# Performance work log

Hardware: AMD Instinct MI355X
Metric: run time of the kernel (lower is better)

The kernel has to match this reference:

```python
import jax, jax.numpy as jnp
import numpy as np

B, S, E, H = 4, 2048, 512, 8
D = E // H  # 64 per-head dim


def setup_inputs() -> dict:
    key = jax.random.key(0)
    kq, kk, kv, kwq, kwk, kwv, kwf, kbf = jax.random.split(key, 8)
    sc = 0.02
    return {
        "query": jax.random.normal(kq, (B, S, E), dtype=jnp.float32),
        "key": jax.random.normal(kk, (B, S, E), dtype=jnp.float32),
        "value": jax.random.normal(kv, (B, S, E), dtype=jnp.float32),
        "Wq": jax.random.normal(kwq, (D, D), dtype=jnp.float32) * sc,
        "Wk": jax.random.normal(kwk, (D, D), dtype=jnp.float32) * sc,
        "Wv": jax.random.normal(kwv, (D, D), dtype=jnp.float32) * sc,
        "Wfc": jax.random.normal(kwf, (E, E), dtype=jnp.float32) * sc,
        "bfc": jnp.zeros((E,), dtype=jnp.float32),
        "mask": jnp.tril(jnp.ones((1, 1, S, S), dtype=jnp.int32)),
    }


def reference(query, key, value, Wq, Wk, Wv, Wfc, bfc, mask):
    b, qlen, _ = query.shape
    klen = key.shape[1]
    # split heads: (B, L, H, D)
    q = query.reshape(b, qlen, H, D)
    k = key.reshape(b, klen, H, D)
    v = value.reshape(b, klen, H, D)
    # per-head linear projections (torch Linear: x @ W.T, no bias)
    q = jnp.einsum('bqhd,ed->bqhe', q, Wq)
    k = jnp.einsum('bkhd,ed->bkhe', k, Wk)
    v = jnp.einsum('bkhd,ed->bkhe', v, Wv)
    # full score matrix (B, H, Q, K)
    scores = jnp.einsum('bqhd,bkhd->bhqk', q, k)
    # faithful to source: mask-fill BEFORE dividing by sqrt(d)
    scores = jnp.where(mask == 0, jnp.float32(-1e20), scores)
    scores = scores / jnp.float32(np.sqrt(D))
    attn = jax.nn.softmax(scores, axis=-1)
    out = jnp.einsum('bhqk,bkhd->bqhd', attn, v).reshape(b, qlen, H * D)
    return out @ Wfc.T + bfc
```

## Files before the change

kernel.cpp:

```cpp
#include <hip/hip_runtime.h>
#include <hip/hip_bf16.h>

#define S_LEN 2048
#define EMB 512
#define NH 8
#define HD 64

#define AS1 __attribute__((address_space(1)))
#define AS3 __attribute__((address_space(3)))

typedef __bf16 bf16x8 __attribute__((ext_vector_type(8)));
typedef __bf16 bf16x4 __attribute__((ext_vector_type(4)));
typedef float f32x4 __attribute__((ext_vector_type(4)));
typedef float f32x16 __attribute__((ext_vector_type(16)));
typedef int i32x4 __attribute__((ext_vector_type(4)));

__device__ __forceinline__ unsigned swz(unsigned byteoff, unsigned row) {
    return byteoff ^ ((row & 7u) << 4);
}

__device__ __forceinline__ bf16x8 cvt8(const float* src) {
    float4 f0 = *reinterpret_cast<const float4*>(src);
    float4 f1 = *reinterpret_cast<const float4*>(src + 4);
    bf16x8 r;
    r[0] = (__bf16)f0.x; r[1] = (__bf16)f0.y; r[2] = (__bf16)f0.z; r[3] = (__bf16)f0.w;
    r[4] = (__bf16)f1.x; r[5] = (__bf16)f1.y; r[6] = (__bf16)f1.z; r[7] = (__bf16)f1.w;
    return r;
}

__global__ __launch_bounds__(256) void wcvt_kernel(
    const float* __restrict__ Wfc, const float* __restrict__ Wq,
    const float* __restrict__ Wk, const float* __restrict__ Wv,
    __bf16* __restrict__ Wb, __bf16* __restrict__ Wf)
{
    if (blockIdx.x < 128) {
        int i = (blockIdx.x * 256 + threadIdx.x) * 8;
        *reinterpret_cast<bf16x8*>(Wb + i) = cvt8(Wfc + i);
    } else {
        int s = (blockIdx.x - 128) * 256 + threadIdx.x;
        int p = s >> 9, rem = s & 511;
        int sub = rem >> 6, l = rem & 63;
        int nf = sub >> 1, ks = sub & 1;
        int col = l & 15, g = l >> 4;
        const float* Wsrc = (p == 0) ? Wq : (p == 1) ? Wk : Wv;
        *reinterpret_cast<bf16x8*>(Wf + (size_t)s * 8) =
            cvt8(Wsrc + (nf * 16 + col) * HD + ks * 32 + g * 8);
    }
}

__global__ __launch_bounds__(256) void proj_kernel(
    const float* __restrict__ qin, const float* __restrict__ kin, const float* __restrict__ vin,
    const __bf16* __restrict__ Wf,
    __bf16* __restrict__ Qf, __bf16* __restrict__ Kf, __bf16* __restrict__ Vf)
{
    __shared__ alignas(16) unsigned char xb[8192];
    __shared__ alignas(16) unsigned char tb[8192];
    const int p = blockIdx.z;
    const int bh = blockIdx.y;
    const int b = bh >> 3, h = bh & 7;
    const int sblk = blockIdx.x << 6;
    const int tid = threadIdx.x;
    const int w = tid >> 6, l = tid & 63;
    const int col = l & 15, g = l >> 4;
    const float K1 = 0.18033688011112042f;

    const float* src = (p == 0 ? qin : p == 1 ? kin : vin) +
                       ((size_t)b * S_LEN + sblk) * EMB + h * HD;
    #pragma unroll
    for (int it = 0; it < 4; ++it) {
        int c = tid + it * 256;
        int row = c >> 4, c4 = c & 15;
        float4 f = *reinterpret_cast<const float4*>(src + (size_t)row * EMB + c4 * 4);
        bf16x4 t;
        t[0] = (__bf16)f.x; t[1] = (__bf16)f.y; t[2] = (__bf16)f.z; t[3] = (__bf16)f.w;
        *reinterpret_cast<bf16x4*>(&xb[swz(row * 128 + c4 * 8, row)]) = t;
    }
    __syncthreads();

    bf16x8 wf[4][2];
    {
        const __bf16* wfb = Wf + p * 4096 + l * 8;
        #pragma unroll
        for (int nf = 0; nf < 4; ++nf)
            #pragma unroll
            for (int ks = 0; ks < 2; ++ks)
                wf[nf][ks] = *reinterpret_cast<const bf16x8*>(wfb + (nf * 2 + ks) * 512);
    }
    int arow = w * 16 + col;
    bf16x8 a0 = *reinterpret_cast<const bf16x8*>(&xb[swz(arow * 128 + g * 16, arow)]);
    bf16x8 a1 = *reinterpret_cast<const bf16x8*>(&xb[swz(arow * 128 + 64 + g * 16, arow)]);
    f32x4 acc[4];
    #pragma unroll
    for (int nf = 0; nf < 4; ++nf) acc[nf] = (f32x4){0.f, 0.f, 0.f, 0.f};
    #pragma unroll
    for (int nf = 0; nf < 4; ++nf) {
        acc[nf] = __builtin_amdgcn_mfma_f32_16x16x32_bf16(a0, wf[nf][0], acc[nf], 0, 0, 0);
        acc[nf] = __builtin_amdgcn_mfma_f32_16x16x32_bf16(a1, wf[nf][1], acc[nf], 0, 0, 0);
    }
    const float s0 = (p == 0) ? K1 : 1.0f;
    #pragma unroll
    for (int nf = 0; nf < 4; ++nf)
        #pragma unroll
        for (int r = 0; r < 4; ++r) {
            int srow = w * 16 + g * 4 + r;
            unsigned tba = (unsigned)(srow * 128 + (nf * 16 + col) * 2) ^ ((srow & 7u) << 4);
            *reinterpret_cast<__bf16*>(&tb[tba]) = (__bf16)(acc[nf][r] * s0);
        }
    __syncthreads();
    if (p < 2) {
        __bf16* dst = (p == 0) ? Qf : Kf;
        #pragma unroll
        for (int it = 0; it < 2; ++it) {
            int s = tid + it * 256;
            int Tloc = s >> 8, ks = (s >> 6) & 3, li = s & 63;
            int c32 = li & 31, h2 = li >> 5;
            int row = Tloc * 32 + c32;
            unsigned tba = (unsigned)(row * 128 + ks * 32 + h2 * 16) ^ ((row & 7u) << 4);
            bf16x8 v = *reinterpret_cast<const bf16x8*>(&tb[tba]);
            *reinterpret_cast<bf16x8*>(
                dst + (size_t)bh * 131072 +
                ((size_t)(blockIdx.x * 2 + Tloc) * 4 + ks) * 512 + li * 8) = v;
        }
    } else {
        #pragma unroll
        for (int it = 0; it < 2; ++it) {
            int s = tid + it * 256;
            int Tloc = s >> 8, sub = (s >> 6) & 3, li = s & 63;
            int nf = sub >> 1, ks2 = sub & 1;
            int c32 = li & 31, h2 = li >> 5;
            int dcol = nf * 32 + c32;
            bf16x8 v;
            #pragma unroll
            for (int e = 0; e < 8; ++e) {
                int row = Tloc * 32 + ks2 * 16 + (e & 3) + 8 * (e >> 2) + 4 * h2;
                unsigned tba = (unsigned)(row * 128 + dcol * 2) ^ ((row & 7u) << 4);
                v[e] = *reinterpret_cast<const __bf16*>(&tb[tba]);
            }
            *reinterpret_cast<bf16x8*>(
                Vf + (size_t)bh * 131072 +
                ((size_t)(blockIdx.x * 2 + Tloc) * 4 + sub) * 512 + li * 8) = v;
        }
    }
}

__global__ __launch_bounds__(256, 4) void attn_kernel(
    const __bf16* __restrict__ Qf, const __bf16* __restrict__ Kf,
    const __bf16* __restrict__ Vf, __bf16* __restrict__ Oa)
{
    __shared__ float mg[2][2112];
    const int l_id = blockIdx.x;
    const int bh = l_id & 31;
    const int pr = l_id >> 5;
    const int b = bh >> 3, h = bh & 7;
    const int tid = threadIdx.x;
    const int kh = tid >> 6;
    const int l = tid & 63;
    const int c32 = l & 31, hi = l >> 5;

    const __bf16* kbase = Kf + (size_t)bh * 131072;
    const __bf16* vbase = Vf + (size_t)bh * 131072;

    #pragma unroll 1
    for (int pass = 0; pass < 2; ++pass) {
        const int qt2 = pass ? 63 - pr : pr;

        bf16x8 qf[4];
        {
            const __bf16* qb = Qf + (size_t)bh * 131072 + (size_t)qt2 * 2048 + l * 8;
            #pragma unroll
            for (int ks = 0; ks < 4; ++ks)
                qf[ks] = *reinterpret_cast<const bf16x8*>(qb + ks * 512);
        }
        f32x16 oacc[2];
        #pragma unroll
        for (int nf = 0; nf < 2; ++nf)
            #pragma unroll
            for (int r = 0; r < 16; ++r) oacc[nf][r] = 0.f;
        float lsum = 0.f;

        const int cnt = (qt2 >= kh) ? ((qt2 - kh) >> 2) + 1 : 0;
        const bool has_mask = (kh == (qt2 & 3));
        const __bf16* kp = kbase + (size_t)kh * 2048 + l * 8;
        const __bf16* vp = vbase + (size_t)kh * 2048 + l * 8;

        #pragma unroll 1
        for (int i = 0; i < cnt; ++i) {
            bf16x8 kcur[4], vcur[4];
            #pragma unroll
            for (int j = 0; j < 4; ++j) {
                kcur[j] = *reinterpret_cast<const bf16x8*>(kp + j * 512);
                vcur[j] = *reinterpret_cast<const bf16x8*>(vp + j * 512);
            }
            f32x16 sfa;
            #pragma unroll
            for (int r = 0; r < 16; ++r) sfa[r] = -16.f;
            #pragma unroll
            for (int ks = 0; ks < 4; ++ks)
                sfa = __builtin_amdgcn_mfma_f32_32x32x16_bf16(kcur[ks], qf[ks], sfa, 0, 0, 0);
            if (has_mask && i == cnt - 1) {
                #pragma unroll
                for (int r = 0; r < 16; ++r) {
                    int kvloc = (r & 3) + 8 * (r >> 2) + 4 * hi;
                    if (kvloc > c32) sfa[r] = -1e30f;
                }
            }
            float rsum = 0.f;
            int wds[8];
            #pragma unroll
            for (int i2 = 0; i2 < 8; ++i2) {
                float p0 = __builtin_exp2f(sfa[2 * i2]);
                float p1 = __builtin_exp2f(sfa[2 * i2 + 1]);
                rsum += p0 + p1;
                asm("v_cvt_pk_bf16_f32 %0, %1, %2" : "=v"(wds[i2]) : "v"(p0), "v"(p1));
            }
            lsum += rsum;
            #pragma unroll
            for (int nf = 0; nf < 2; ++nf) {
                #pragma unroll
                for (int ks2 = 0; ks2 < 2; ++ks2) {
                    i32x4 pw;
                    pw[0] = wds[ks2 * 4 + 0];
                    pw[1] = wds[ks2 * 4 + 1];
                    pw[2] = wds[ks2 * 4 + 2];
                    pw[3] = wds[ks2 * 4 + 3];
                    bf16x8 pfk = *reinterpret_cast<bf16x8*>(&pw);
                    oacc[nf] = __builtin_amdgcn_mfma_f32_32x32x16_bf16(
                        vcur[nf * 2 + ks2], pfk, oacc[nf], 0, 0, 0);
                }
            }
            kp += 8192;
            vp += 8192;
        }

        __syncthreads();
        if (kh & 1) {
            float* bp = mg[kh >> 1];
            #pragma unroll
            for (int nf = 0; nf < 2; ++nf)
                #pragma unroll
                for (int r = 0; r < 16; ++r)
                    bp[(nf * 16 + r) * 64 + l] = oacc[nf][r];
            bp[2048 + l] = lsum;
        }
        __syncthreads();
        if (!(kh & 1)) {
            const float* bp = mg[kh >> 1];
            lsum += bp[2048 + l];
            #pragma unroll
            for (int nf = 0; nf < 2; ++nf)
                #pragma unroll
                for (int r = 0; r < 16; ++r)
                    oacc[nf][r] += bp[(nf * 16 + r) * 64 + l];
        }
        __syncthreads();
        if (kh == 2) {
            float* bp = mg[0];
            #pragma unroll
            for (int nf = 0; nf < 2; ++nf)
                #pragma unroll
                for (int r = 0; r < 16; ++r)
                    bp[(nf * 16 + r) * 64 + l] = oacc[nf][r];
            bp[2048 + l] = lsum;
        }
        __syncthreads();
        if (kh == 0) {
            const float* bp = mg[0];
            lsum += bp[2048 + l];
            #pragma unroll
            for (int nf = 0; nf < 2; ++nf)
                #pragma unroll
                for (int r = 0; r < 16; ++r)
                    oacc[nf][r] += bp[(nf * 16 + r) * 64 + l];
            lsum += __shfl_xor(lsum, 32);
            float inv = 1.0f / lsum;
            const int q = qt2 * 32 + c32;
            __bf16* op = Oa + ((size_t)b * S_LEN + q) * EMB + h * HD;
            #pragma unroll
            for (int nf = 0; nf < 2; ++nf)
                #pragma unroll
                for (int rq = 0; rq < 4; ++rq) {
                    bf16x4 o4;
                    #pragma unroll
                    for (int e = 0; e < 4; ++e)
                        o4[e] = (__bf16)(oacc[nf][rq * 4 + e] * inv);
                    *reinterpret_cast<bf16x4*>(op + nf * 32 + rq * 8 + hi * 4) = o4;
                }
        }
    }
}

__global__ __launch_bounds__(512) void fc_kernel(
    const __bf16* __restrict__ A,
    const __bf16* __restrict__ Wb,
    const float* __restrict__ bfc,
    float* __restrict__ out)
{
    __shared__ alignas(16) unsigned char smem[65536];
    const int tid = threadIdx.x;
    const int w = tid >> 6, l = tid & 63;
    const int c32 = l & 31, hi = l >> 5;
    const int mw = w >> 2, nw = w & 3;
    const int r0 = blockIdx.x * 128, n0 = blockIdx.y * 128;

    int sro[2], sof[2];
    #pragma unroll
    for (int j = 0; j < 2; ++j) {
        int s = w * 128 + j * 64 + l;
        int row = s >> 3, off = (s & 7) * 16;
        sro[j] = row;
        sof[j] = off ^ ((row & 7) << 4);
    }
    const unsigned char* Ag = reinterpret_cast<const unsigned char*>(A) + (size_t)r0 * 1024;
    const unsigned char* Wg = reinterpret_cast<const unsigned char*>(Wb) + (size_t)n0 * 1024;

    f32x16 oacc[2];
    #pragma unroll
    for (int nf = 0; nf < 2; ++nf)
        #pragma unroll
        for (int r = 0; r < 16; ++r) oacc[nf][r] = 0.f;

    #pragma unroll
    for (int j = 0; j < 2; ++j) {
        __builtin_amdgcn_global_load_lds(
            (const AS1 unsigned int*)(Ag + (size_t)sro[j] * 1024 + sof[j]),
            (AS3 unsigned int*)(smem + w * 2048 + j * 1024), 16, 0, 0);
        __builtin_amdgcn_global_load_lds(
            (const AS1 unsigned int*)(Wg + (size_t)sro[j] * 1024 + sof[j]),
            (AS3 unsigned int*)(smem + 16384 + w * 2048 + j * 1024), 16, 0, 0);
    }
    __syncthreads();

    int cur = 0;
    #pragma unroll 1
    for (int kc = 0; kc < 8; ++kc) {
        if (kc + 1 < 8) {
            unsigned char* Abn = smem + (cur ^ 1) * 32768;
            #pragma unroll
            for (int j = 0; j < 2; ++j) {
                __builtin_amdgcn_global_load_lds(
                    (const AS1 unsigned int*)(Ag + (size_t)sro[j] * 1024 + (kc + 1) * 128 + sof[j]),
                    (AS3 unsigned int*)(Abn + w * 2048 + j * 1024), 16, 0, 0);
                __builtin_amdgcn_global_load_lds(
                    (const AS1 unsigned int*)(Wg + (size_t)sro[j] * 1024 + (kc + 1) * 128 + sof[j]),
                    (AS3 unsigned int*)(Abn + 16384 + w * 2048 + j * 1024), 16, 0, 0);
            }
        }
        unsigned char* Ab = smem + cur * 32768;
        unsigned char* Wbuf = Ab + 16384;
        const int brow = nw * 32 + c32;
        #pragma unroll
        for (int ks = 0; ks < 4; ++ks) {
            bf16x8 bfg = *reinterpret_cast<const bf16x8*>(
                Wbuf + swz(brow * 128 + ks * 32 + hi * 16, brow));
            #pragma unroll
            for (int nf = 0; nf < 2; ++nf) {
                int arow = mw * 64 + nf * 32 + c32;
                bf16x8 afg = *reinterpret_cast<const bf16x8*>(
                    Ab + swz(arow * 128 + ks * 32 + hi * 16, arow));
                oacc[nf] = __builtin_amdgcn_mfma_f32_32x32x16_bf16(afg, bfg, oacc[nf], 0, 0, 0);
            }
        }
        __syncthreads();
        cur ^= 1;
    }

    const float bias = bfc[n0 + nw * 32 + c32];
    const int ncol = n0 + nw * 32 + c32;
    #pragma unroll
    for (int nf = 0; nf < 2; ++nf)
        #pragma unroll
        for (int r = 0; r < 16; ++r) {
            int mrow = r0 + mw * 64 + nf * 32 + (r & 3) + 8 * (r >> 2) + 4 * hi;
            out[(size_t)mrow * EMB + ncol] = oacc[nf][r] + bias;
        }
}

extern "C" void kernel_launch(void* const* d_in, const int* in_sizes, int n_in,
                              void* d_out, int out_size, void* d_ws, size_t ws_size,
                              hipStream_t stream) {
    const float* q   = (const float*)d_in[0];
    const float* k   = (const float*)d_in[1];
    const float* v   = (const float*)d_in[2];
    const float* Wq  = (const float*)d_in[3];
    const float* Wk  = (const float*)d_in[4];
    const float* Wv  = (const float*)d_in[5];
    const float* Wfc = (const float*)d_in[6];
    const float* bfc = (const float*)d_in[7];
    float* out = (float*)d_out;

    char* ws = (char*)d_ws;
    const size_t SZ = (size_t)4 * NH * S_LEN * HD * sizeof(__bf16);
    __bf16* Qf = (__bf16*)(ws);
    __bf16* Kf = (__bf16*)(ws + SZ);
    __bf16* Vf = (__bf16*)(ws + 2 * SZ);
    __bf16* Oa = (__bf16*)(ws + 3 * SZ);
    __bf16* Wb = (__bf16*)(ws + 4 * SZ);
    __bf16* Wf = (__bf16*)(ws + 4 * SZ + 524288);

    wcvt_kernel<<<dim3(134), 256, 0, stream>>>(Wfc, Wq, Wk, Wv, Wb, Wf);
    proj_kernel<<<dim3(S_LEN / 64, 4 * NH, 3), 256, 0, stream>>>(q, k, v, Wf, Qf, Kf, Vf);
    attn_kernel<<<dim3(32 * 32), 256, 0, stream>>>(Qf, Kf, Vf, Oa);
    fc_kernel<<<dim3((4 * S_LEN) / 128, EMB / 128), 512, 0, stream>>>(Oa, Wb, bfc, out);
}
```

Before: 66.45 us.

## Fuse paired causal query tiles into one KV loop sharing K/V loads

The attention kernel now processes both paired query tiles (pr and 63-pr) in a single loop over KV blocks instead of two sequential passes. Each loaded K/V fragment is reused for both tiles, roughly halving global K/V traffic for the shorter tile and removing a second loop prologue. This doubles Q-fragment and accumulator register use, so launch bounds drop from 4 to 3 waves per SIMD, which lowers occupancy and latency hiding. The merge/epilogue loop then indexes the two accumulator sets through a pointer, which may force register arrays into scratch memory.

```diff
diff --git a/kernel.cpp b/kernel.cpp
--- a/kernel.cpp
+++ b/kernel.cpp
@@ -143,7 +143,7 @@
     }
 }
 
-__global__ __launch_bounds__(256, 4) void attn_kernel(
+__global__ __launch_bounds__(256, 3) void attn_kernel(
     const __bf16* __restrict__ Qf, const __bf16* __restrict__ Kf,
     const __bf16* __restrict__ Vf, __bf16* __restrict__ Oa)
 {
@@ -157,81 +157,122 @@
     const int l = tid & 63;
     const int c32 = l & 31, hi = l >> 5;
 
-    const __bf16* kbase = Kf + (size_t)bh * 131072;
-    const __bf16* vbase = Vf + (size_t)bh * 131072;
+    const int qtA = pr, qtB = 63 - pr;
+
+    bf16x8 qfA[4], qfB[4];
+    {
+        const __bf16* qa = Qf + (size_t)bh * 131072 + (size_t)qtA * 2048 + l * 8;
+        const __bf16* qb = Qf + (size_t)bh * 131072 + (size_t)qtB * 2048 + l * 8;
+        #pragma unroll
+        for (int ks = 0; ks < 4; ++ks) {
+            qfA[ks] = *reinterpret_cast<const bf16x8*>(qa + ks * 512);
+            qfB[ks] = *reinterpret_cast<const bf16x8*>(qb + ks * 512);
+        }
+    }
+    f32x16 oaccA[2], oaccB[2];
+    #pragma unroll
+    for (int nf = 0; nf < 2; ++nf)
+        #pragma unroll
+        for (int r = 0; r < 16; ++r) { oaccA[nf][r] = 0.f; oaccB[nf][r] = 0.f; }
+    float lsumA = 0.f, lsumB = 0.f;
+
+    const int cntA = (qtA >= kh) ? ((qtA - kh) >> 2) + 1 : 0;
+    const int cntB = ((qtB - kh) >> 2) + 1;
+    const bool maskA = (kh == (qtA & 3));
+    const bool maskB = (kh == (qtB & 3));
+    const __bf16* kp = Kf + (size_t)bh * 131072 + (size_t)kh * 2048 + l * 8;
+    const __bf16* vp = Vf + (size_t)bh * 131072 + (size_t)kh * 2048 + l * 8;
 
     #pragma unroll 1
-    for (int pass = 0; pass < 2; ++pass) {
-        const int qt2 = pass ? 63 - pr : pr;
-
-        bf16x8 qf[4];
+    for (int i = 0; i < cntB; ++i) {
+        bf16x8 kcur[4], vcur[4];
+        #pragma unroll
+        for (int j = 0; j < 4; ++j) {
+            kcur[j] = *reinterpret_cast<const bf16x8*>(kp + j * 512);
+            vcur[j] = *reinterpret_cast<const bf16x8*>(vp + j * 512);
+        }
+        f32x16 sfa;
+        #pragma unroll
+        for (int r = 0; r < 16; ++r) sfa[r] = -16.f;
+        #pragma unroll
+        for (int ks = 0; ks < 4; ++ks)
+            sfa = __builtin_amdgcn_mfma_f32_32x32x16_bf16(kcur[ks], qfB[ks], sfa, 0, 0, 0);
+        if (maskB && i == cntB - 1) {
+            #pragma unroll
+            for (int r = 0; r < 16; ++r) {
+                int kvloc = (r & 3) + 8 * (r >> 2) + 4 * hi;
+                if (kvloc > c32) sfa[r] = -1e30f;
+            }
+        }
+        int wdsB[8];
         {
-            const __bf16* qb = Qf + (size_t)bh * 131072 + (size_t)qt2 * 2048 + l * 8;
+            float rsum = 0.f;
+            #pragma unroll
+            for (int i2 = 0; i2 < 8; ++i2) {
+                float p0 = __builtin_exp2f(sfa[2 * i2]);
+                float p1 = __builtin_exp2f(sfa[2 * i2 + 1]);
+                rsum += p0 + p1;
+                asm("v_cvt_pk_bf16_f32 %0, %1, %2" : "=v"(wdsB[i2]) : "v"(p0), "v"(p1));
+            }
+            lsumB += rsum;
+        }
+        #pragma unroll
+        for (int nf = 0; nf < 2; ++nf)
+            #pragma unroll
+            for (int ks2 = 0; ks2 < 2; ++ks2) {
+                i32x4 pw;
+                pw[0] = wdsB[ks2 * 4 + 0]; pw[1] = wdsB[ks2 * 4 + 1];
+                pw[2] = wdsB[ks2 * 4 + 2]; pw[3] = wdsB[ks2 * 4 + 3];
+                bf16x8 pfk = *reinterpret_cast<bf16x8*>(&pw);
+                oaccB[nf] = __builtin_amdgcn_mfma_f32_32x32x16_bf16(
+                    vcur[nf * 2 + ks2], pfk, oaccB[nf], 0, 0, 0);
+            }
+        if (i < cntA) {
+            #pragma unroll
+            for (int r = 0; r < 16; ++r) sfa[r] = -16.f;
             #pragma unroll
             for (int ks = 0; ks < 4; ++ks)
-                qf[ks] = *reinterpret_cast<const bf16x8*>(qb + ks * 512);
-        }
-        f32x16 oacc[2];
-        #pragma unroll
-        for (int nf = 0; nf < 2; ++nf)
-            #pragma unroll
-            for (int r = 0; r < 16; ++r) oacc[nf][r] = 0.f;
-        float lsum = 0.f;
-
-        const int cnt = (qt2 >= kh) ? ((qt2 - kh) >> 2) + 1 : 0;
-        const bool has_mask = (kh == (qt2 & 3));
-        const __bf16* kp = kbase + (size_t)kh * 2048 + l * 8;
-        const __bf16* vp = vbase + (size_t)kh * 2048 + l * 8;
-
-        #pragma unroll 1
-        for (int i = 0; i < cnt; ++i) {
-            bf16x8 kcur[4], vcur[4];
-            #pragma unroll
-            for (int j = 0; j < 4; ++j) {
-                kcur[j] = *reinterpret_cast<const bf16x8*>(kp + j * 512);
-                vcur[j] = *reinterpret_cast<const bf16x8*>(vp + j * 512);
-            }
-            f32x16 sfa;
-            #pragma unroll
-            for (int r = 0; r < 16; ++r) sfa[r] = -16.f;
-            #pragma unroll
-            for (int ks = 0; ks < 4; ++ks)
-                sfa = __builtin_amdgcn_mfma_f32_32x32x16_bf16(kcur[ks], qf[ks], sfa, 0, 0, 0);
-            if (has_mask && i == cnt - 1) {
+                sfa = __builtin_amdgcn_mfma_f32_32x32x16_bf16(kcur[ks], qfA[ks], sfa, 0, 0, 0);
+            if (maskA && i == cntA - 1) {
                 #pragma unroll
                 for (int r = 0; r < 16; ++r) {
                     int kvloc = (r & 3) + 8 * (r >> 2) + 4 * hi;
                     if (kvloc > c32) sfa[r] = -1e30f;
                 }
             }
-            float rsum = 0.f;
-            int wds[8];
-            #pragma unroll
-            for (int i2 = 0; i2 < 8; ++i2) {
-                float p0 = __builtin_exp2f(sfa[2 * i2]);
-                float p1 = __builtin_exp2f(sfa[2 * i2 + 1]);
-                rsum += p0 + p1;
-                asm("v_cvt_pk_bf16_f32 %0, %1, %2" : "=v"(wds[i2]) : "v"(p0), "v"(p1));
-            }
-            lsum += rsum;
-            #pragma unroll
-            for (int nf = 0; nf < 2; ++nf) {
+            int wdsA[8];
+            {
+                float rsum = 0.f;
+                #pragma unroll
+                for (int i2 = 0; i2 < 8; ++i2) {
+                    float p0 = __builtin_exp2f(sfa[2 * i2]);
+                    float p1 = __builtin_exp2f(sfa[2 * i2 + 1]);
+                    rsum += p0 + p1;
+                    asm("v_cvt_pk_bf16_f32 %0, %1, %2" : "=v"(wdsA[i2]) : "v"(p0), "v"(p1));
+                }
+                lsumA += rsum;
+            }
+            #pragma unroll
+            for (int nf = 0; nf < 2; ++nf)
                 #pragma unroll
                 for (int ks2 = 0; ks2 < 2; ++ks2) {
                     i32x4 pw;
-                    pw[0] = wds[ks2 * 4 + 0];
-                    pw[1] = wds[ks2 * 4 + 1];
-                    pw[2] = wds[ks2 * 4 + 2];
-                    pw[3] = wds[ks2 * 4 + 3];
+                    pw[0] = wdsA[ks2 * 4 + 0]; pw[1] = wdsA[ks2 * 4 + 1];
+                    pw[2] = wdsA[ks2 * 4 + 2]; pw[3] = wdsA[ks2 * 4 + 3];
                     bf16x8 pfk = *reinterpret_cast<bf16x8*>(&pw);
-                    oacc[nf] = __builtin_amdgcn_mfma_f32_32x32x16_bf16(
-                        vcur[nf * 2 + ks2], pfk, oacc[nf], 0, 0, 0);
+                    oaccA[nf] = __builtin_amdgcn_mfma_f32_32x32x16_bf16(
+                        vcur[nf * 2 + ks2], pfk, oaccA[nf], 0, 0, 0);
                 }
-            }
-            kp += 8192;
-            vp += 8192;
-        }
-
+        }
+        kp += 8192;
+        vp += 8192;
+    }
+
+    #pragma unroll 1
+    for (int ps = 0; ps < 2; ++ps) {
+        const int qt2 = ps ? qtB : qtA;
+        f32x16* oacc = ps ? oaccB : oaccA;
+        float lsum = ps ? lsumB : lsumA;
         __syncthreads();
         if (kh & 1) {
             float* bp = mg[kh >> 1];
```

Result: slower. 116.1 us (+74.7%).
